# Kernel optimization log

Measured on AMD Instinct MI355X. Metric: run time of the kernel, lower is better.

## Reference

```python
import jax, jax.numpy as jnp
import numpy as np

D_MODEL = 1024
NUM_TILES = 64
TPC = 8                      # tiles_per_cluster
NUM_CLUSTERS = NUM_TILES // TPC
GRID = 16
COMP_H = 256                 # compress hidden = d_model // 4
NUM_KNOTS = 8
EPS_LN = 1e-5


def setup_inputs() -> dict:
    key = jax.random.key(0)
    ks = jax.random.split(key, 12)
    B, T = 4, 4096
    x = jax.random.normal(ks[0], (B, T, D_MODEL), dtype=jnp.float32)
    signatures_raw = jax.random.normal(ks[1], (NUM_TILES, D_MODEL), dtype=jnp.float32) * 0.5
    knot_values = jax.nn.sigmoid(jnp.linspace(-3.0, 3.0, NUM_KNOTS).astype(jnp.float32))
    temperature = jnp.ones((1,), dtype=jnp.float32)
    # compress: Linear(d,comp_h) -> GELU -> Linear(comp_h,2) -> Tanh
    compress_w1 = jax.random.normal(ks[2], (D_MODEL, COMP_H), dtype=jnp.float32) * (1.0 / np.sqrt(D_MODEL))
    compress_b1 = jnp.zeros((COMP_H,), dtype=jnp.float32)
    compress_w2 = jax.random.normal(ks[3], (COMP_H, 2), dtype=jnp.float32) * (1.0 / np.sqrt(COMP_H))
    compress_b2 = jnp.zeros((2,), dtype=jnp.float32)
    # per-tile magnitude splines: Linear(2,grid) -> ReLU -> Linear(grid,1)
    spline_w1 = jax.random.normal(ks[4], (NUM_TILES, 2, GRID), dtype=jnp.float32) * (1.0 / np.sqrt(2.0))
    spline_b1 = jnp.zeros((NUM_TILES, GRID), dtype=jnp.float32)
    spline_w2 = jax.random.normal(ks[5], (NUM_TILES, GRID, 1), dtype=jnp.float32) * (1.0 / np.sqrt(GRID))
    spline_b2 = jnp.zeros((NUM_TILES, 1), dtype=jnp.float32)
    directions = jax.random.normal(ks[6], (NUM_TILES, D_MODEL), dtype=jnp.float32) * 0.02
    norm_gamma = jnp.ones((D_MODEL,), dtype=jnp.float32)
    norm_beta = jnp.zeros((D_MODEL,), dtype=jnp.float32)
    output_scale = jnp.ones((1,), dtype=jnp.float32) * 0.1
    return dict(x=x, signatures_raw=signatures_raw, knot_values=knot_values,
                temperature=temperature, compress_w1=compress_w1, compress_b1=compress_b1,
                compress_w2=compress_w2, compress_b2=compress_b2, spline_w1=spline_w1,
                spline_b1=spline_b1, spline_w2=spline_w2, spline_b2=spline_b2,
                directions=directions, norm_gamma=norm_gamma, norm_beta=norm_beta,
                output_scale=output_scale)


def _calibrate(scores, knots, temperature):
    # ScoreCalibrationSpline: sigmoid -> linear interpolation over knots
    K = knots.shape[0]
    normalized = jax.nn.sigmoid(scores / (temperature[0] + 1e-6))
    idx_float = normalized * (K - 1)
    idx_low = jnp.clip(idx_float.astype(jnp.int32), 0, K - 2)
    idx_high = idx_low + 1
    t = idx_float - idx_low.astype(scores.dtype)
    val_low = knots[idx_low]
    val_high = knots[idx_high]
    return val_low + t * (val_high - val_low)


def _forward(x, signatures_raw, knot_values, temperature, compress_w1, compress_b1,
             compress_w2, compress_b2, spline_w1, spline_b1, spline_w2, spline_b2,
             directions, norm_gamma, norm_beta, output_scale):
    B, T, D = x.shape
    xf = x.reshape(-1, D)  # [N, D]

    # ternary quantized signatures with straight-through estimator
    q = jnp.where(signatures_raw > 0.3, 1.0,
                  jnp.where(signatures_raw < -0.3, -1.0, 0.0)).astype(signatures_raw.dtype)
    sigs = signatures_raw + jax.lax.stop_gradient(q - signatures_raw)  # [NT, D]

    # hierarchical routing: cluster signatures = sign(mean of member sigs)
    cluster_sigs = jnp.sign(sigs.reshape(NUM_CLUSTERS, TPC, D).mean(axis=1))  # [NC, D]
    cluster_scores = xf @ cluster_sigs.T                                       # [N, NC]
    cluster_gates = _calibrate(cluster_scores, knot_values, temperature)
    cluster_idx = jnp.argmax(cluster_gates, axis=-1)                           # [N]

    # within-cluster tile selection (clusters are contiguous blocks of tiles)
    tile_scores = xf @ sigs.T                                                  # [N, NT]
    tile_gates = _calibrate(tile_scores, knot_values, temperature)
    gates_by_cluster = tile_gates.reshape(-1, NUM_CLUSTERS, TPC)
    sel_gates = jnp.take_along_axis(gates_by_cluster, cluster_idx[:, None, None],
                                    axis=1)[:, 0, :]                            # [N, TPC]
    local_idx = jnp.argmax(sel_gates, axis=-1)
    tile_idx = cluster_idx * TPC + local_idx                                    # [N]

    # compress to 2D spline coordinates
    h = jax.nn.gelu(xf @ compress_w1 + compress_b1, approximate=False)
    comp = jnp.tanh(h @ compress_w2 + compress_b2)                              # [N, 2]

    # batched per-token tiny spline MLP (gather selected tile's weights)
    w1 = spline_w1[tile_idx]                                                    # [N, 2, G]
    b1 = spline_b1[tile_idx]                                                    # [N, G]
    hh = jax.nn.relu(jnp.einsum('ni,nig->ng', comp, w1) + b1)                   # [N, G]
    w2 = spline_w2[tile_idx]                                                    # [N, G, 1]
    b2 = spline_b2[tile_idx]                                                    # [N, 1]
    mag = jnp.einsum('ng,ngo->no', hh, w2) + b2                                 # [N, 1]

    ffn_out = mag * directions[tile_idx] * output_scale[0]                      # [N, D]

    # residual + LayerNorm (dropout in eval mode = identity)
    y = xf + ffn_out
    mu = y.mean(axis=-1, keepdims=True)
    var = ((y - mu) ** 2).mean(axis=-1, keepdims=True)
    y = (y - mu) / jnp.sqrt(var + EPS_LN) * norm_gamma + norm_beta
    return y.reshape(B, T, D)


def reference(x, signatures_raw, knot_values, temperature, compress_w1, compress_b1,
              compress_w2, compress_b2, spline_w1, spline_b1, spline_w2, spline_b2,
              directions, norm_gamma, norm_beta, output_scale):
    return _forward(x, signatures_raw, knot_values, temperature, compress_w1, compress_b1,
                    compress_w2, compress_b2, spline_w1, spline_b1, spline_w2, spline_b2,
                    directions, norm_gamma, norm_beta, output_scale)
```

## Files before the change

### kernel.cpp

```cpp
#include <hip/hip_runtime.h>
#include <hip/hip_bf16.h>
#include <cmath>

#define N_TOK 16384
#define DM    1024
#define CH    256
#define SGRID 16
#define NTP   24

typedef __attribute__((ext_vector_type(8))) short short8;
typedef __attribute__((ext_vector_type(4))) float floatx4;

__device__ __forceinline__ unsigned short f2bf(float f) {
  union { float f; unsigned int u; } v; v.f = f;
  unsigned int r = v.u + 0x7FFFu + ((v.u >> 16) & 1u);
  return (unsigned short)(r >> 16);
}

__device__ __forceinline__ short8 cvt8(float4 u, float4 v) {
  union { short8 s; __hip_bfloat162 h[4]; } r;
  r.h[0] = __float22bfloat162_rn(make_float2(u.x, u.y));
  r.h[1] = __float22bfloat162_rn(make_float2(u.z, u.w));
  r.h[2] = __float22bfloat162_rn(make_float2(v.x, v.y));
  r.h[3] = __float22bfloat162_rn(make_float2(v.z, v.w));
  return r.s;
}

__device__ __forceinline__ float bf2f(unsigned short b) {
  union { unsigned int u; float f; } v; v.u = ((unsigned int)b) << 16; return v.f;
}

__device__ __forceinline__ float calibrate(float s, const float* __restrict__ kn, float temp_eff) {
  float nrm = 1.0f / (1.0f + expf(-s / temp_eff));
  float idxf = nrm * 7.0f;
  int il = (int)idxf; if (il > 6) il = 6;
  float tt = idxf - (float)il;
  float lo = kn[il], hi = kn[il + 1];
  return lo + tt * (hi - lo);
}

__global__ __launch_bounds__(256) void prep_kernel(
    const float* __restrict__ sig_raw, const float* __restrict__ w1,
    unsigned short* __restrict__ wsB) {
  __shared__ float Wt[32][260];
  __shared__ float St[64][33];
  int kk = blockIdx.x, tid = threadIdx.x;
  {
    int r = tid >> 3, c0 = (tid & 7) * 32;
    const float* src = w1 + (size_t)(kk * 32 + r) * CH + c0;
#pragma unroll
    for (int i = 0; i < 8; ++i)
      *(float4*)(&Wt[r][c0 + 4 * i]) = *(const float4*)(src + 4 * i);
  }
  {
    int t = tid >> 2, c0 = (tid & 3) * 8;
    const float* src = sig_raw + (size_t)t * DM + kk * 32 + c0;
#pragma unroll
    for (int i = 0; i < 8; ++i) {
      float rr = src[i];
      St[t][c0 + i] = (rr > 0.3f) ? 1.f : ((rr < -0.3f) ? -1.f : 0.f);
    }
  }
  __syncthreads();
#pragma unroll
  for (int i = 0; i < 4; ++i) {
    int idx = i * 256 + tid;
    int nt = idx >> 6, lane = idx & 63;
    int q = lane >> 4, l = lane & 15;
    short8 v;
#pragma unroll
    for (int j = 0; j < 8; ++j) v[j] = (short)f2bf(Wt[q * 8 + j][nt * 16 + l]);
    *(short8*)(wsB + ((size_t)(kk * NTP + nt) * 64 + lane) * 8) = v;
  }
#pragma unroll
  for (int i = 0; i < 2; ++i) {
    int idx = i * 256 + tid;
    if (idx < 320) {
      int nt = 16 + (idx >> 6), lane = idx & 63;
      int q = lane >> 4, l = lane & 15;
      int n = nt * 16 + l;
      short8 v;
#pragma unroll
      for (int j = 0; j < 8; ++j) {
        int kl = q * 8 + j;
        float val = 0.f;
        if (n < 264) {
          float s = 0.f;
#pragma unroll
          for (int m = 0; m < 8; ++m) s += St[(n - 256) * 8 + m][kl];
          val = (s > 0.f) ? 1.f : ((s < 0.f) ? -1.f : 0.f);
        } else if (n < 328) {
          val = St[n - 264][kl];
        }
        v[j] = (short)f2bf(val);
      }
      *(short8*)(wsB + ((size_t)(kk * NTP + nt) * 64 + lane) * 8) = v;
    }
  }
}


#define LOADK(kk, b0, b1, av)                                               \
  {                                                                         \
    const char* bp = bBase + (size_t)(kk) * (NTP * 1024);                   \
    b0 = *(const short8*)(bp);                                              \
    if (wave < 5) b1 = *(const short8*)(bp + 16384);                        \
    unsigned cpos = ((unsigned)((kk) * 4 + quad) ^ sw) << 3;                \
    _Pragma("unroll") for (int mt = 0; mt < 4; ++mt)                        \
        av[mt] = *(const short8*)(Xsh + mt * 16384 + arow + cpos);          \
  }

#define COMPUTE(b0, b1, av)                                                 \
  {                                                                         \
    _Pragma("unroll") for (int mt = 0; mt < 4; ++mt)                        \
      acc0[mt] = __builtin_amdgcn_mfma_f32_16x16x32_bf16(av[mt], b0, acc0[mt], 0, 0, 0); \
    if (wave < 5) {                                                         \
      _Pragma("unroll") for (int mt = 0; mt < 4; ++mt)                      \
        acc1[mt] = __builtin_amdgcn_mfma_f32_16x16x32_bf16(av[mt], b1, acc1[mt], 0, 0, 0); \
    }                                                                       \
  }

__global__ __launch_bounds__(1024, 4) void fused_kernel(
    const float* __restrict__ x, const unsigned short* __restrict__ wsB,
    const float* __restrict__ b1v, const float* __restrict__ w2,
    const float* __restrict__ b2, const float* __restrict__ knots,
    const float* __restrict__ temperature, const float* __restrict__ sw1,
    const float* __restrict__ sb1, const float* __restrict__ sw2,
    const float* __restrict__ sb2, const float* __restrict__ dirs,
    const float* __restrict__ gma, const float* __restrict__ bta,
    const float* __restrict__ oscale, float* __restrict__ out) {
  __shared__ unsigned short Xsh[64 * 1024];
  __shared__ float Ssc[64][73];
  __shared__ float Psh[16][64][2];
  __shared__ float ScaleS[64];
  __shared__ int   TidxS[64];

  int tid = threadIdx.x;
  int wave = tid >> 6, lane = tid & 63, quad = lane >> 4, l15 = lane & 15;
  int m0 = blockIdx.x * 64;

  {
    const float* base = x + (size_t)m0 * DM;
#pragma unroll
    for (int i2 = 0; i2 < 8; ++i2) {
      int cg = tid + 1024 * i2;
      float4 p = *(const float4*)(base + cg * 8);
      float4 q = *(const float4*)(base + cg * 8 + 4);
      int row = cg >> 7, cir = cg & 127;
      int pos = cir ^ (row & 7);
      *(short8*)(Xsh + row * 1024 + pos * 8) = cvt8(p, q);
    }
  }
  __syncthreads();

  floatx4 acc0[4], acc1[4];
#pragma unroll
  for (int mt = 0; mt < 4; ++mt) {
    acc0[mt] = (floatx4){0.f, 0.f, 0.f, 0.f};
    acc1[mt] = (floatx4){0.f, 0.f, 0.f, 0.f};
  }

  const char* bBase = (const char*)wsB + wave * 1024 + lane * 16;
  int arow = l15 * 1024;
  unsigned sw = (unsigned)(l15 & 7);

  short8 bA0, bA1, bB0, bB1, aA[4], aB_[4];
  LOADK(0, bA0, bA1, aA);
#pragma unroll 1
  for (int kk = 0; kk < 30; kk += 2) {
    LOADK(kk + 1, bB0, bB1, aB_);
    COMPUTE(bA0, bA1, aA);
    LOADK(kk + 2, bA0, bA1, aA);
    COMPUTE(bB0, bB1, aB_);
  }
  LOADK(31, bB0, bB1, aB_);
  COMPUTE(bA0, bA1, aA);
  COMPUTE(bB0, bB1, aB_);

  if (wave < 5) {
    int sc = wave * 16 + l15;
    if (sc < 72) {
#pragma unroll
      for (int mt = 0; mt < 4; ++mt)
#pragma unroll
        for (int r = 0; r < 4; ++r)
          Ssc[mt * 16 + quad * 4 + r][sc] = acc1[mt][r];
    }
  }

  {
    int col = wave * 16 + l15;
    float b1c = b1v[col], w20 = w2[2 * col], w21 = w2[2 * col + 1];
    float q0[4][4], q1[4][4];
#pragma unroll
    for (int mt = 0; mt < 4; ++mt)
#pragma unroll
      for (int r = 0; r < 4; ++r) {
        float hh = acc0[mt][r] + b1c;
        hh = 0.5f * hh * (1.0f + erff(hh * 0.7071067811865475f));
        q0[mt][r] = hh * w20;
        q1[mt][r] = hh * w21;
      }
#pragma unroll
    for (int m = 1; m < 16; m <<= 1)
#pragma unroll
      for (int mt = 0; mt < 4; ++mt)
#pragma unroll
        for (int r = 0; r < 4; ++r) {
          q0[mt][r] += __shfl_xor(q0[mt][r], m);
          q1[mt][r] += __shfl_xor(q1[mt][r], m);
        }
    if (l15 == 0) {
#pragma unroll
      for (int mt = 0; mt < 4; ++mt)
#pragma unroll
        for (int r = 0; r < 4; ++r) {
          Psh[wave][mt * 16 + quad * 4 + r][0] = q0[mt][r];
          Psh[wave][mt * 16 + quad * 4 + r][1] = q1[mt][r];
        }
    }
  }
  __syncthreads();

  if (tid < 64) {
    int row = tid;
    float s0 = b2[0], s1 = b2[1];
#pragma unroll
    for (int j = 0; j < 16; ++j) {
      s0 += Psh[j][row][0];
      s1 += Psh[j][row][1];
    }
    float c0 = tanhf(s0), c1 = tanhf(s1);

    float temp_eff = temperature[0] + 1e-6f;
    int cid = 0; float best = -1e30f;
#pragma unroll
    for (int c = 0; c < 8; ++c) {
      float g = calibrate(Ssc[row][c], knots, temp_eff);
      if (g > best) { best = g; cid = c; }
    }
    int lidx = 0; best = -1e30f;
#pragma unroll
    for (int j = 0; j < 8; ++j) {
      float g = calibrate(Ssc[row][8 + cid * 8 + j], knots, temp_eff);
      if (g > best) { best = g; lidx = j; }
    }
    int t = cid * 8 + lidx;

    float mag = sb2[t];
#pragma unroll
    for (int g2 = 0; g2 < SGRID; ++g2) {
      float hv = c0 * sw1[t * 32 + g2] + c1 * sw1[t * 32 + 16 + g2] + sb1[t * 16 + g2];
      hv = fmaxf(hv, 0.f);
      mag += hv * sw2[t * 16 + g2];
    }
    ScaleS[row] = mag * oscale[0];
    TidxS[row] = t;
  }
  __syncthreads();

#pragma unroll 1
  for (int rr = 0; rr < 4; ++rr) {
    int row = wave * 4 + rr;
    int r7 = row & 7;
    float scale = ScaleS[row];
    const float* dr = dirs + (size_t)TidxS[row] * DM + lane * 16;
    const unsigned short* xrow = Xsh + row * 1024;
    short8 h0 = *(const short8*)(xrow + (unsigned)((2 * lane) ^ r7) * 8);
    short8 h1 = *(const short8*)(xrow + (unsigned)((2 * lane + 1) ^ r7) * 8);
    float fv[16];
    float ssum = 0.f, ssq = 0.f;
#pragma unroll
    for (int i = 0; i < 4; ++i) {
      float4 d4 = *(const float4*)(dr + 4 * i);
      float xa = bf2f((unsigned short)((i < 2 ? h0[i * 4 + 0] : h1[(i - 2) * 4 + 0])));
      float xb = bf2f((unsigned short)((i < 2 ? h0[i * 4 + 1] : h1[(i - 2) * 4 + 1])));
      float xc = bf2f((unsigned short)((i < 2 ? h0[i * 4 + 2] : h1[(i - 2) * 4 + 2])));
      float xd = bf2f((unsigned short)((i < 2 ? h0[i * 4 + 3] : h1[(i - 2) * 4 + 3])));
      fv[4 * i + 0] = xa + scale * d4.x;
      fv[4 * i + 1] = xb + scale * d4.y;
      fv[4 * i + 2] = xc + scale * d4.z;
      fv[4 * i + 3] = xd + scale * d4.w;
      ssum += fv[4 * i + 0] + fv[4 * i + 1] + fv[4 * i + 2] + fv[4 * i + 3];
      ssq += fv[4 * i + 0] * fv[4 * i + 0] + fv[4 * i + 1] * fv[4 * i + 1]
           + fv[4 * i + 2] * fv[4 * i + 2] + fv[4 * i + 3] * fv[4 * i + 3];
    }
#pragma unroll
    for (int m = 1; m < 64; m <<= 1) {
      ssum += __shfl_xor(ssum, m);
      ssq += __shfl_xor(ssq, m);
    }
    float mu = ssum * (1.0f / 1024.0f);
    float var = ssq * (1.0f / 1024.0f) - mu * mu;
    float inv = rsqrtf(var + 1e-5f);
    float* orow = out + (size_t)(m0 + row) * DM + lane * 16;
    const float* gp = gma + lane * 16;
    const float* bp2 = bta + lane * 16;
#pragma unroll
    for (int i = 0; i < 4; ++i) {
      float4 g4 = *(const float4*)(gp + 4 * i);
      float4 b4 = *(const float4*)(bp2 + 4 * i);
      float4 o;
      o.x = (fv[4 * i + 0] - mu) * inv * g4.x + b4.x;
      o.y = (fv[4 * i + 1] - mu) * inv * g4.y + b4.y;
      o.z = (fv[4 * i + 2] - mu) * inv * g4.z + b4.z;
      o.w = (fv[4 * i + 3] - mu) * inv * g4.w + b4.w;
      *(float4*)(orow + 4 * i) = o;
    }
  }
}

extern "C" void kernel_launch(void* const* d_in, const int* in_sizes, int n_in,
                              void* d_out, int out_size, void* d_ws, size_t ws_size,
                              hipStream_t stream) {
  const float* x      = (const float*)d_in[0];
  const float* sigraw = (const float*)d_in[1];
  const float* knots  = (const float*)d_in[2];
  const float* temp   = (const float*)d_in[3];
  const float* cw1    = (const float*)d_in[4];
  const float* cb1    = (const float*)d_in[5];
  const float* cw2    = (const float*)d_in[6];
  const float* cb2    = (const float*)d_in[7];
  const float* sw1    = (const float*)d_in[8];
  const float* sb1    = (const float*)d_in[9];
  const float* sw2    = (const float*)d_in[10];
  const float* sb2    = (const float*)d_in[11];
  const float* dirs   = (const float*)d_in[12];
  const float* gma    = (const float*)d_in[13];
  const float* bta    = (const float*)d_in[14];
  const float* oscale = (const float*)d_in[15];
  float* out = (float*)d_out;

  unsigned short* wsB = (unsigned short*)d_ws;

  hipLaunchKernelGGL(prep_kernel, dim3(32), dim3(256), 0, stream,
                     sigraw, cw1, wsB);
  hipLaunchKernelGGL(fused_kernel, dim3(N_TOK / 64), dim3(1024), 0, stream,
                     x, wsB, cb1, cw2, cb2, knots, temp,
                     sw1, sb1, sw2, sb2, dirs, gma, bta, oscale, out);
}
```

Baseline: 174.5 us.

## Pipeline X tile staging into LDS with the MFMA K-loop in groups

Instead of loading and converting the whole 64x1024 x tile into shared memory before the GEMM, the kernel now stages it in eight column groups of 128. Each group's global loads are prefetched while the previous group is converted, then a barrier precedes four MFMA k-steps over that group. The aim is to overlap the global load latency of x with tensor-core work. In exchange it adds eight block barriers and removes the double-buffered register prefetch of B/A fragments, so each LOADK is consumed immediately and its latency may be exposed.

```diff
diff --git a/kernel.cpp b/kernel.cpp
--- a/kernel.cpp
+++ b/kernel.cpp
@@ -117,6 +117,23 @@
     if (wave < 5) {                                                         \
       _Pragma("unroll") for (int mt = 0; mt < 4; ++mt)                      \
         acc1[mt] = __builtin_amdgcn_mfma_f32_16x16x32_bf16(av[mt], b1, acc1[mt], 0, 0, 0); \
+    }                                                                       \
+  }
+
+#define GROUP(g, XA, XB, YA, YB)                                            \
+  {                                                                         \
+    if ((g) < 7) {                                                          \
+      YA = *(const float4*)(xsrc + ((g) + 1) * 128);                        \
+      YB = *(const float4*)(xsrc + ((g) + 1) * 128 + 4);                    \
+    }                                                                       \
+    *(short8*)(xdst + ((unsigned)((g) * 16 + scc) ^ ssw) * 8) = cvt8(XA, XB); \
+    asm volatile("s_waitcnt lgkmcnt(0)" ::: "memory");                      \
+    __builtin_amdgcn_s_barrier();                                           \
+    __builtin_amdgcn_sched_barrier(0);                                      \
+    _Pragma("unroll") for (int k4 = 0; k4 < 4; ++k4) {                      \
+      int kk = (g) * 4 + k4;                                                \
+      LOADK(kk, bA0, bA1, aA);                                              \
+      COMPUTE(bA0, bA1, aA);                                                \
     }                                                                       \
   }
 
@@ -139,19 +156,10 @@
   int wave = tid >> 6, lane = tid & 63, quad = lane >> 4, l15 = lane & 15;
   int m0 = blockIdx.x * 64;
 
-  {
-    const float* base = x + (size_t)m0 * DM;
-#pragma unroll
-    for (int i2 = 0; i2 < 8; ++i2) {
-      int cg = tid + 1024 * i2;
-      float4 p = *(const float4*)(base + cg * 8);
-      float4 q = *(const float4*)(base + cg * 8 + 4);
-      int row = cg >> 7, cir = cg & 127;
-      int pos = cir ^ (row & 7);
-      *(short8*)(Xsh + row * 1024 + pos * 8) = cvt8(p, q);
-    }
-  }
-  __syncthreads();
+  int srow = tid >> 4, scc = tid & 15;
+  const float* xsrc = x + (size_t)(m0 + srow) * DM + scc * 8;
+  unsigned short* xdst = Xsh + srow * 1024;
+  unsigned ssw = (unsigned)(srow & 7);
 
   floatx4 acc0[4], acc1[4];
 #pragma unroll
@@ -163,19 +171,19 @@
   const char* bBase = (const char*)wsB + wave * 1024 + lane * 16;
   int arow = l15 * 1024;
   unsigned sw = (unsigned)(l15 & 7);
-
-  short8 bA0, bA1, bB0, bB1, aA[4], aB_[4];
-  LOADK(0, bA0, bA1, aA);
-#pragma unroll 1
-  for (int kk = 0; kk < 30; kk += 2) {
-    LOADK(kk + 1, bB0, bB1, aB_);
-    COMPUTE(bA0, bA1, aA);
-    LOADK(kk + 2, bA0, bA1, aA);
-    COMPUTE(bB0, bB1, aB_);
-  }
-  LOADK(31, bB0, bB1, aB_);
-  COMPUTE(bA0, bA1, aA);
-  COMPUTE(bB0, bB1, aB_);
+  short8 bA0, bA1, aA[4];
+
+  float4 xa0, xb0, xa1, xb1;
+  xa0 = *(const float4*)(xsrc);
+  xb0 = *(const float4*)(xsrc + 4);
+  GROUP(0, xa0, xb0, xa1, xb1);
+  GROUP(1, xa1, xb1, xa0, xb0);
+  GROUP(2, xa0, xb0, xa1, xb1);
+  GROUP(3, xa1, xb1, xa0, xb0);
+  GROUP(4, xa0, xb0, xa1, xb1);
+  GROUP(5, xa1, xb1, xa0, xb0);
+  GROUP(6, xa0, xb0, xa1, xb1);
+  GROUP(7, xa1, xb1, xa0, xb0);
 
   if (wave < 5) {
     int sc = wave * 16 + l15;
```

Result: no change. 177.5 us (+1.7%).

## Concentrate GEMM on six waves with four N-tiles each for A-fragment reuse

Applied to the files above, without the earlier changes.

The projection GEMM previously spread 21 N-tiles over 16 waves, with each wave doing one or two tiles and reloading the A fragments from LDS per tile. Now only six waves compute, each owning four N-tiles, so one set of A fragments from LDS feeds 16 MFMAs per k-step. This cuts LDS traffic and partial-sum reductions (Psh shrinks from 16 to 4 slices). The trade-off is that ten waves sit idle during the GEMM and each active wave holds more accumulator registers, so latency hiding and parallelism may suffer. The explicit double-buffered load macros are also dropped in favour of a simple unrolled loop.

```diff
diff --git a/kernel.cpp b/kernel.cpp
--- a/kernel.cpp
+++ b/kernel.cpp
@@ -99,26 +99,6 @@
   }
 }
 
-
-#define LOADK(kk, b0, b1, av)                                               \
-  {                                                                         \
-    const char* bp = bBase + (size_t)(kk) * (NTP * 1024);                   \
-    b0 = *(const short8*)(bp);                                              \
-    if (wave < 5) b1 = *(const short8*)(bp + 16384);                        \
-    unsigned cpos = ((unsigned)((kk) * 4 + quad) ^ sw) << 3;                \
-    _Pragma("unroll") for (int mt = 0; mt < 4; ++mt)                        \
-        av[mt] = *(const short8*)(Xsh + mt * 16384 + arow + cpos);          \
-  }
-
-#define COMPUTE(b0, b1, av)                                                 \
-  {                                                                         \
-    _Pragma("unroll") for (int mt = 0; mt < 4; ++mt)                        \
-      acc0[mt] = __builtin_amdgcn_mfma_f32_16x16x32_bf16(av[mt], b0, acc0[mt], 0, 0, 0); \
-    if (wave < 5) {                                                         \
-      _Pragma("unroll") for (int mt = 0; mt < 4; ++mt)                      \
-        acc1[mt] = __builtin_amdgcn_mfma_f32_16x16x32_bf16(av[mt], b1, acc1[mt], 0, 0, 0); \
-    }                                                                       \
-  }
 
 __global__ __launch_bounds__(1024, 4) void fused_kernel(
     const float* __restrict__ x, const unsigned short* __restrict__ wsB,
@@ -131,7 +111,7 @@
     const float* __restrict__ oscale, float* __restrict__ out) {
   __shared__ unsigned short Xsh[64 * 1024];
   __shared__ float Ssc[64][73];
-  __shared__ float Psh[16][64][2];
+  __shared__ float Psh[4][64][2];
   __shared__ float ScaleS[64];
   __shared__ int   TidxS[64];
 
@@ -153,70 +133,97 @@
   }
   __syncthreads();
 
-  floatx4 acc0[4], acc1[4];
-#pragma unroll
-  for (int mt = 0; mt < 4; ++mt) {
-    acc0[mt] = (floatx4){0.f, 0.f, 0.f, 0.f};
-    acc1[mt] = (floatx4){0.f, 0.f, 0.f, 0.f};
-  }
-
-  const char* bBase = (const char*)wsB + wave * 1024 + lane * 16;
   int arow = l15 * 1024;
   unsigned sw = (unsigned)(l15 & 7);
 
-  short8 bA0, bA1, bB0, bB1, aA[4], aB_[4];
-  LOADK(0, bA0, bA1, aA);
-#pragma unroll 1
-  for (int kk = 0; kk < 30; kk += 2) {
-    LOADK(kk + 1, bB0, bB1, aB_);
-    COMPUTE(bA0, bA1, aA);
-    LOADK(kk + 2, bA0, bA1, aA);
-    COMPUTE(bB0, bB1, aB_);
-  }
-  LOADK(31, bB0, bB1, aB_);
-  COMPUTE(bA0, bA1, aA);
-  COMPUTE(bB0, bB1, aB_);
-
-  if (wave < 5) {
-    int sc = wave * 16 + l15;
-    if (sc < 72) {
+  floatx4 acc[4][4];
+  if (wave < 6) {
+#pragma unroll
+    for (int i = 0; i < 4; ++i)
+#pragma unroll
+      for (int mt = 0; mt < 4; ++mt)
+        acc[i][mt] = (floatx4){0.f, 0.f, 0.f, 0.f};
+
+    int tB = (wave < 4) ? wave * 4 : (wave == 4) ? 16 : 19;
+    const char* bBase = (const char*)wsB + tB * 1024 + lane * 16;
+#pragma unroll 2
+    for (int kk = 0; kk < 32; ++kk) {
+      const char* bp = bBase + (size_t)kk * (NTP * 1024);
+      short8 bv[4], av[4];
+#pragma unroll
+      for (int i = 0; i < 4; ++i) bv[i] = *(const short8*)(bp + i * 1024);
+      unsigned cpos = ((unsigned)(kk * 4 + quad) ^ sw) << 3;
+#pragma unroll
+      for (int mt = 0; mt < 4; ++mt)
+        av[mt] = *(const short8*)(Xsh + mt * 16384 + arow + cpos);
+#pragma unroll
+      for (int i = 0; i < 4; ++i)
+#pragma unroll
+        for (int mt = 0; mt < 4; ++mt)
+          acc[i][mt] = __builtin_amdgcn_mfma_f32_16x16x32_bf16(av[mt], bv[i], acc[i][mt], 0, 0, 0);
+    }
+  }
+
+  if (wave == 4) {
+#pragma unroll
+    for (int i = 0; i < 3; ++i) {
+      int sc = i * 16 + l15;
 #pragma unroll
       for (int mt = 0; mt < 4; ++mt)
 #pragma unroll
         for (int r = 0; r < 4; ++r)
-          Ssc[mt * 16 + quad * 4 + r][sc] = acc1[mt][r];
-    }
-  }
-
-  {
-    int col = wave * 16 + l15;
-    float b1c = b1v[col], w20 = w2[2 * col], w21 = w2[2 * col + 1];
-    float q0[4][4], q1[4][4];
+          Ssc[mt * 16 + quad * 4 + r][sc] = acc[i][mt][r];
+    }
+  } else if (wave == 5) {
+#pragma unroll
+    for (int i = 0; i < 2; ++i) {
+      int sc = 48 + i * 16 + l15;
+      if (sc < 72) {
+#pragma unroll
+        for (int mt = 0; mt < 4; ++mt)
+#pragma unroll
+          for (int r = 0; r < 4; ++r)
+            Ssc[mt * 16 + quad * 4 + r][sc] = acc[i][mt][r];
+      }
+    }
+  }
+
+  if (wave < 4) {
+    float p0[4][4], p1[4][4];
 #pragma unroll
     for (int mt = 0; mt < 4; ++mt)
 #pragma unroll
-      for (int r = 0; r < 4; ++r) {
-        float hh = acc0[mt][r] + b1c;
-        hh = 0.5f * hh * (1.0f + erff(hh * 0.7071067811865475f));
-        q0[mt][r] = hh * w20;
-        q1[mt][r] = hh * w21;
-      }
+      for (int r = 0; r < 4; ++r) { p0[mt][r] = 0.f; p1[mt][r] = 0.f; }
+#pragma unroll
+    for (int i = 0; i < 4; ++i) {
+      int col = wave * 64 + i * 16 + l15;
+      float b1c = b1v[col], w20 = w2[2 * col], w21 = w2[2 * col + 1];
+#pragma unroll
+      for (int mt = 0; mt < 4; ++mt)
+#pragma unroll
+        for (int r = 0; r < 4; ++r) {
+          float hh = acc[i][mt][r] + b1c;
+          hh = 0.5f * hh * (1.0f + erff(hh * 0.7071067811865475f));
+          p0[mt][r] += hh * w20;
+          p1[mt][r] += hh * w21;
+        }
+    }
 #pragma unroll
     for (int m = 1; m < 16; m <<= 1)
 #pragma unroll
       for (int mt = 0; mt < 4; ++mt)
 #pragma unroll
         for (int r = 0; r < 4; ++r) {
-          q0[mt][r] += __shfl_xor(q0[mt][r], m);
-          q1[mt][r] += __shfl_xor(q1[mt][r], m);
+          p0[mt][r] += __shfl_xor(p0[mt][r], m);
+          p1[mt][r] += __shfl_xor(p1[mt][r], m);
         }
     if (l15 == 0) {
 #pragma unroll
       for (int mt = 0; mt < 4; ++mt)
 #pragma unroll
         for (int r = 0; r < 4; ++r) {
-          Psh[wave][mt * 16 + quad * 4 + r][0] = q0[mt][r];
-          Psh[wave][mt * 16 + quad * 4 + r][1] = q1[mt][r];
+          Psh[wave][mt * 16 + quad * 4 + r][0] = p0[mt][r];
+          Psh[wave][mt * 16 + quad * 4 + r][1] = p1[mt][r];
         }
     }
   }
@@ -226,7 +233,7 @@
     int row = tid;
     float s0 = b2[0], s1 = b2[1];
 #pragma unroll
-    for (int j = 0; j < 16; ++j) {
+    for (int j = 0; j < 4; ++j) {
       s0 += Psh[j][row][0];
       s1 += Psh[j][row][1];
     }
```

Result: slower. 213.2 us (+22.2%).
